# Kernel optimization log

Measured on AMD Instinct MI355X. Metric: run time of the kernel, lower is better.

## Reference

```python
import jax, jax.numpy as jnp
import numpy as np

N_NODES = 50000
N_EDGES = 800000
K_HOPS = 3


def setup_inputs() -> dict:
    key = jax.random.key(0)
    ks = jax.random.split(key, 8)
    x = jax.random.normal(ks[0], (N_NODES, 56), dtype=jnp.float32)
    edge_index = jax.random.randint(ks[1], (2, N_EDGES), 0, N_NODES, dtype=jnp.int64)
    def glorot(k, shape):
        fan_in, fan_out = shape
        s = (6.0 / (fan_in + fan_out)) ** 0.5
        return jax.random.uniform(k, shape, jnp.float32, -s, s)
    return {
        "x": x,
        "edge_index": edge_index,
        "W1": glorot(ks[2], (56, 64)), "b1": jnp.zeros((64,), jnp.float32),
        "W2": glorot(ks[3], (64, 64)), "b2": jnp.zeros((64,), jnp.float32),
        "W3": glorot(ks[4], (64, 64)), "b3": jnp.zeros((64,), jnp.float32),
        "W4": glorot(ks[5], (64, 256)), "b4": jnp.zeros((256,), jnp.float32),
    }


def _gcn_norm(edge_index, num_nodes, dtype):
    # add self loops (PyG SGConv default), then symmetric D^{-1/2}(A+I)D^{-1/2} weights
    loop = jnp.arange(num_nodes, dtype=edge_index.dtype)
    src = jnp.concatenate([edge_index[0], loop])
    dst = jnp.concatenate([edge_index[1], loop])
    deg = jax.ops.segment_sum(jnp.ones_like(src, dtype=dtype), dst, num_segments=num_nodes)
    dinv = jnp.where(deg > 0, jax.lax.rsqrt(deg), 0.0).astype(dtype)
    norm = dinv[src] * dinv[dst]  # [E + N]
    return src, dst, norm


def _propagate_k(h, src, dst, norm, num_nodes, k):
    # k hops of sparse gather-scale-scatter: h <- A_hat @ h
    for _ in range(k):
        h = jax.ops.segment_sum(h[src] * norm[:, None], dst, num_segments=num_nodes)
    return h


def reference(x, edge_index, W1, b1, W2, b2, W3, b3, W4, b4):
    n = x.shape[0]
    src, dst, norm = _gcn_norm(edge_index, n, x.dtype)
    # SGConv layers (dropout is identity in eval mode)
    h = _propagate_k(x, src, dst, norm, n, K_HOPS) @ W1 + b1
    h = _propagate_k(h, src, dst, norm, n, K_HOPS) @ W2 + b2
    h = _propagate_k(h, src, dst, norm, n, K_HOPS) @ W3 + b3
    return h @ W4 + b4  # [N, output]
```

## Files before the change

### kernel.cpp

```cpp
#include <hip/hip_runtime.h>

#define N_NODES 50000
#define N_EDGES 800000
#define F_IN 56
#define F_PAD 64
#define F_OUT 256
#define NB 64
#define ELL_W 64


__global__ void k_fill(const int* __restrict__ ei, int* __restrict__ cnt,
                       int* __restrict__ ell) {
  int e = blockIdx.x * blockDim.x + threadIdx.x;
  if (e >= N_EDGES) return;
  int s = ei[e];
  int d = ei[N_EDGES + e];
  int pos = atomicAdd(&cnt[d], 1);
  ell[(d << 6) + pos] = s;
}


__global__ void k_dinv(const int* __restrict__ cnt, float* __restrict__ dinv,
                       int* __restrict__ deg, int* __restrict__ ell) {
  int i = blockIdx.x * blockDim.x + threadIdx.x;
  if (i >= N_NODES) return;
  int c = cnt[i];
  dinv[i] = rsqrtf((float)(c + 1));
  deg[i] = c + 1;
  ell[(i << 6) + c] = i;
}


__global__ void k_loadx(const float* __restrict__ x, float* __restrict__ h) {
  int i = blockIdx.x * blockDim.x + threadIdx.x;
  int nn = i >> 6, f = i & 63;
  float v = 0.f;
  if (f < F_IN) v = x[nn * F_IN + f];
  else if (f == F_IN) v = 1.f;
  h[i] = v;
}


__global__ __launch_bounds__(256) void k_hop(const float* __restrict__ hin,
                                             float* __restrict__ hout,
                                             const int* __restrict__ deg,
                                             const int* __restrict__ ell,
                                             const float* __restrict__ dinv,
                                             float* __restrict__ vsave) {
  int node = (blockIdx.x * blockDim.x + threadIdx.x) >> 6;
  int lane = threadIdx.x & 63;
  int d = __builtin_amdgcn_readfirstlane(deg[node]);
  int rec = ell[((size_t)node << 6) + lane];
  rec = (lane < d) ? rec : node;
  float dn = __int_as_float(__builtin_amdgcn_readfirstlane(
      __float_as_int(dinv[node])));
  float wl = (lane < d) ? dinv[rec] * dn : 0.f;

  int sub = lane >> 4;
  int fo  = (lane & 15) << 2;
  float4 acc = make_float4(0.f, 0.f, 0.f, 0.f);

  int ngroups = (d + 3) >> 2;
  int g = 0;
  for (; g + 2 <= ngroups; g += 2) {
    int   s0 = __shfl(rec, g * 4 + sub);
    float w0 = __shfl(wl,  g * 4 + sub);
    int   s1 = __shfl(rec, g * 4 + 4 + sub);
    float w1 = __shfl(wl,  g * 4 + 4 + sub);
    float4 a0 = *(const float4*)(hin + (((size_t)s0) << 6) + fo);
    float4 a1 = *(const float4*)(hin + (((size_t)s1) << 6) + fo);
    acc.x = fmaf(w0, a0.x, acc.x);
    acc.y = fmaf(w0, a0.y, acc.y);
    acc.z = fmaf(w0, a0.z, acc.z);
    acc.w = fmaf(w0, a0.w, acc.w);
    acc.x = fmaf(w1, a1.x, acc.x);
    acc.y = fmaf(w1, a1.y, acc.y);
    acc.z = fmaf(w1, a1.z, acc.z);
    acc.w = fmaf(w1, a1.w, acc.w);
  }
  if (g < ngroups) {
    int   s0 = __shfl(rec, g * 4 + sub);
    float w0 = __shfl(wl,  g * 4 + sub);
    float4 a0 = *(const float4*)(hin + (((size_t)s0) << 6) + fo);
    acc.x = fmaf(w0, a0.x, acc.x);
    acc.y = fmaf(w0, a0.y, acc.y);
    acc.z = fmaf(w0, a0.z, acc.z);
    acc.w = fmaf(w0, a0.w, acc.w);
  }
  acc.x += __shfl_xor(acc.x, 16);
  acc.y += __shfl_xor(acc.y, 16);
  acc.z += __shfl_xor(acc.z, 16);
  acc.w += __shfl_xor(acc.w, 16);
  acc.x += __shfl_xor(acc.x, 32);
  acc.y += __shfl_xor(acc.y, 32);
  acc.z += __shfl_xor(acc.z, 32);
  acc.w += __shfl_xor(acc.w, 32);

  if (lane < 16) {
    *(float4*)(hout + ((size_t)node << 6) + fo) = acc;
  }
  if (vsave != nullptr && lane == 14) vsave[node] = acc.x;
}


__global__ void k_weights(const float* __restrict__ W1, const float* __restrict__ b1,
                          const float* __restrict__ W2, const float* __restrict__ b2,
                          const float* __restrict__ W3, const float* __restrict__ b3,
                          const float* __restrict__ W4, const float* __restrict__ b4,
                          float* __restrict__ Mw, float* __restrict__ c1,
                          float* __restrict__ c2, float* __restrict__ c3) {
  __shared__ float t1[64], t2[64], t3[64];
  int m = blockIdx.x, tid = threadIdx.x;
  if (m < F_IN) {
    if (tid < 64) {
      float a = 0.f;
      for (int k = 0; k < 64; ++k) a = fmaf(W1[m * 64 + k], W2[k * 64 + tid], a);
      t1[tid] = a;
    }
    __syncthreads();
    if (tid < 64) {
      float a = 0.f;
      for (int k = 0; k < 64; ++k) a = fmaf(t1[k], W3[k * 64 + tid], a);
      t2[tid] = a;
    }
    __syncthreads();
    {
      float a = 0.f;
      for (int k = 0; k < 64; ++k) a = fmaf(t2[k], W4[k * 256 + tid], a);
      Mw[m * 256 + tid] = a;
    }
  } else {
    if (tid < 64) {
      float a = 0.f;
      for (int k = 0; k < 64; ++k) a = fmaf(b1[k], W2[k * 64 + tid], a);
      t1[tid] = a;
    }
    __syncthreads();
    if (tid < 64) {
      float a = 0.f, b = 0.f;
      for (int k = 0; k < 64; ++k) {
        float w3 = W3[k * 64 + tid];
        a = fmaf(t1[k], w3, a);
        b = fmaf(b2[k], w3, b);
      }
      t2[tid] = a; t3[tid] = b;
    }
    __syncthreads();
    {
      float a = 0.f, b = 0.f, c = 0.f;
      for (int k = 0; k < 64; ++k) {
        float w4 = W4[k * 256 + tid];
        a = fmaf(t2[k], w4, a);
        b = fmaf(t3[k], w4, b);
        c = fmaf(b3[k], w4, c);
      }
      c1[tid] = a; c2[tid] = b; c3[tid] = c + b4[tid];
    }
  }
}


__global__ __launch_bounds__(256) void k_final(const float* __restrict__ y,
                                               const float* __restrict__ v3,
                                               const float* __restrict__ v6,
                                               const float* __restrict__ Mw,
                                               const float* __restrict__ c1,
                                               const float* __restrict__ c2,
                                               const float* __restrict__ c3,
                                               float* __restrict__ out) {
  __shared__ float4 yl[NB][16];
  __shared__ float v3l[NB], v6l[NB];
  int tid = threadIdx.x;
  int j = tid;

  float4 Mreg[14];
#pragma unroll
  for (int k4 = 0; k4 < 14; ++k4) {
    Mreg[k4].x = Mw[(k4 * 4 + 0) * F_OUT + j];
    Mreg[k4].y = Mw[(k4 * 4 + 1) * F_OUT + j];
    Mreg[k4].z = Mw[(k4 * 4 + 2) * F_OUT + j];
    Mreg[k4].w = Mw[(k4 * 4 + 3) * F_OUT + j];
  }
  float C1 = c1[j], C2 = c2[j], C3 = c3[j];

  int n0 = blockIdx.x * NB;
  int lim = min(NB, N_NODES - n0);
  for (int i = tid; i < lim * 16; i += 256) {
    int nn = i >> 4, q = i & 15;
    yl[nn][q] = *(const float4*)(y + ((size_t)(n0 + nn) << 6) + q * 4);
  }
  if (tid < lim) { v3l[tid] = v3[n0 + tid]; v6l[tid] = v6[n0 + tid]; }
  __syncthreads();

  for (int nn = 0; nn < lim; ++nn) {
    float acc = fmaf(v6l[nn], C1, fmaf(v3l[nn], C2, C3));
#pragma unroll
    for (int k4 = 0; k4 < 14; ++k4) {
      float4 yv = yl[nn][k4];
      acc = fmaf(yv.x, Mreg[k4].x, acc);
      acc = fmaf(yv.y, Mreg[k4].y, acc);
      acc = fmaf(yv.z, Mreg[k4].z, acc);
      acc = fmaf(yv.w, Mreg[k4].w, acc);
    }
    out[(size_t)(n0 + nn) * F_OUT + j] = acc;
  }
}


extern "C" void kernel_launch(void* const* d_in, const int* in_sizes, int n_in,
                              void* d_out, int out_size, void* d_ws, size_t ws_size,
                              hipStream_t stream) {
  const float* x  = (const float*)d_in[0];
  const int*   ei = (const int*)d_in[1];
  const float* W1 = (const float*)d_in[2];
  const float* b1 = (const float*)d_in[3];
  const float* W2 = (const float*)d_in[4];
  const float* b2 = (const float*)d_in[5];
  const float* W3 = (const float*)d_in[6];
  const float* b3 = (const float*)d_in[7];
  const float* W4 = (const float*)d_in[8];
  const float* b4 = (const float*)d_in[9];
  float* out = (float*)d_out;

  char* ws = (char*)d_ws;
  size_t off = 0;
  auto take = [&](size_t bytes) -> void* {
    void* p = ws + off;
    off += (bytes + 255) & ~(size_t)255;
    return p;
  };
  int*   cnt   = (int*)take((size_t)N_NODES * 4);
  int*   deg   = (int*)take((size_t)N_NODES * 4);
  float* dinv  = (float*)take((size_t)N_NODES * 4);
  float* v3    = (float*)take((size_t)N_NODES * 4);
  float* v6    = (float*)take((size_t)N_NODES * 4);
  int*   ell   = (int*)take((size_t)N_NODES * ELL_W * 4);
  float* hA    = (float*)take((size_t)N_NODES * F_PAD * 4);
  float* hB    = (float*)take((size_t)N_NODES * F_PAD * 4);
  float* Mw    = (float*)take((size_t)F_IN * F_OUT * 4);
  float* c1    = (float*)take((size_t)F_OUT * 4);
  float* c2    = (float*)take((size_t)F_OUT * 4);
  float* c3    = (float*)take((size_t)F_OUT * 4);

  (void)hipMemsetAsync(cnt, 0, (size_t)N_NODES * 4, stream);
  k_fill<<<(N_EDGES + 255) / 256, 256, 0, stream>>>(ei, cnt, ell);
  k_dinv<<<(N_NODES + 255) / 256, 256, 0, stream>>>(cnt, dinv, deg, ell);
  k_loadx<<<(N_NODES * F_PAD) / 256, 256, 0, stream>>>(x, hA);
  k_weights<<<F_IN + 1, 256, 0, stream>>>(W1, b1, W2, b2, W3, b3, W4, b4, Mw, c1, c2, c3);

  float* src = hA;
  float* dst = hB;
  for (int hop = 1; hop <= 9; ++hop) {
    float* vs = (hop == 3) ? v3 : (hop == 6) ? v6 : nullptr;
    k_hop<<<(N_NODES * F_PAD) / 256, 256, 0, stream>>>(src, dst, deg, ell, dinv, vs);
    float* t = src; src = dst; dst = t;
  }
  k_final<<<(N_NODES + NB - 1) / NB, 256, 0, stream>>>(src, v3, v6, Mw, c1, c2, c3, out);
}
```

Baseline: 386.1 us.

## Partition ELL fill by destination segment, unroll hop gather, dual-row final GEMV

The ELL build now runs as a fixed grid of blocks, each handling only the destination nodes in one of eight segments. This is meant to localise atomics and ELL writes per XCD/cache region, but every block rereads all destination indices. The hop gather loop is unrolled to four neighbour groups so more loads are in flight. The final projection processes two nodes per iteration with split accumulators and halves the block node count to improve ILP and grid size.

```diff
diff --git a/kernel.cpp b/kernel.cpp
--- a/kernel.cpp
+++ b/kernel.cpp
@@ -5,18 +5,26 @@
 #define F_IN 56
 #define F_PAD 64
 #define F_OUT 256
-#define NB 64
+#define NB 32
 #define ELL_W 64
-
-
-__global__ void k_fill(const int* __restrict__ ei, int* __restrict__ cnt,
-                       int* __restrict__ ell) {
-  int e = blockIdx.x * blockDim.x + threadIdx.x;
-  if (e >= N_EDGES) return;
-  int s = ei[e];
-  int d = ei[N_EDGES + e];
-  int pos = atomicAdd(&cnt[d], 1);
-  ell[(d << 6) + pos] = s;
+#define SEG_SZ 6250
+
+
+__global__ __launch_bounds__(256) void k_fill(const int* __restrict__ ei,
+                                              int* __restrict__ cnt,
+                                              int* __restrict__ ell) {
+  int seg = blockIdx.x & 7;
+  int chunk = blockIdx.x >> 3;
+  int nchunks = gridDim.x >> 3;
+  int stride = nchunks * blockDim.x;
+  for (int e = chunk * blockDim.x + threadIdx.x; e < N_EDGES; e += stride) {
+    int d = ei[N_EDGES + e];
+    if (d / SEG_SZ == seg) {
+      int s = ei[e];
+      int pos = atomicAdd(&cnt[d], 1);
+      ell[(d << 6) + pos] = s;
+    }
+  }
 }
 
 
@@ -62,30 +70,34 @@
 
   int ngroups = (d + 3) >> 2;
   int g = 0;
-  for (; g + 2 <= ngroups; g += 2) {
+  for (; g + 4 <= ngroups; g += 4) {
     int   s0 = __shfl(rec, g * 4 + sub);
     float w0 = __shfl(wl,  g * 4 + sub);
     int   s1 = __shfl(rec, g * 4 + 4 + sub);
     float w1 = __shfl(wl,  g * 4 + 4 + sub);
+    int   s2 = __shfl(rec, g * 4 + 8 + sub);
+    float w2 = __shfl(wl,  g * 4 + 8 + sub);
+    int   s3 = __shfl(rec, g * 4 + 12 + sub);
+    float w3 = __shfl(wl,  g * 4 + 12 + sub);
     float4 a0 = *(const float4*)(hin + (((size_t)s0) << 6) + fo);
     float4 a1 = *(const float4*)(hin + (((size_t)s1) << 6) + fo);
-    acc.x = fmaf(w0, a0.x, acc.x);
-    acc.y = fmaf(w0, a0.y, acc.y);
-    acc.z = fmaf(w0, a0.z, acc.z);
-    acc.w = fmaf(w0, a0.w, acc.w);
-    acc.x = fmaf(w1, a1.x, acc.x);
-    acc.y = fmaf(w1, a1.y, acc.y);
-    acc.z = fmaf(w1, a1.z, acc.z);
-    acc.w = fmaf(w1, a1.w, acc.w);
-  }
-  if (g < ngroups) {
+    float4 a2 = *(const float4*)(hin + (((size_t)s2) << 6) + fo);
+    float4 a3 = *(const float4*)(hin + (((size_t)s3) << 6) + fo);
+    acc.x = fmaf(w0, a0.x, acc.x); acc.y = fmaf(w0, a0.y, acc.y);
+    acc.z = fmaf(w0, a0.z, acc.z); acc.w = fmaf(w0, a0.w, acc.w);
+    acc.x = fmaf(w1, a1.x, acc.x); acc.y = fmaf(w1, a1.y, acc.y);
+    acc.z = fmaf(w1, a1.z, acc.z); acc.w = fmaf(w1, a1.w, acc.w);
+    acc.x = fmaf(w2, a2.x, acc.x); acc.y = fmaf(w2, a2.y, acc.y);
+    acc.z = fmaf(w2, a2.z, acc.z); acc.w = fmaf(w2, a2.w, acc.w);
+    acc.x = fmaf(w3, a3.x, acc.x); acc.y = fmaf(w3, a3.y, acc.y);
+    acc.z = fmaf(w3, a3.z, acc.z); acc.w = fmaf(w3, a3.w, acc.w);
+  }
+  for (; g < ngroups; ++g) {
     int   s0 = __shfl(rec, g * 4 + sub);
     float w0 = __shfl(wl,  g * 4 + sub);
     float4 a0 = *(const float4*)(hin + (((size_t)s0) << 6) + fo);
-    acc.x = fmaf(w0, a0.x, acc.x);
-    acc.y = fmaf(w0, a0.y, acc.y);
-    acc.z = fmaf(w0, a0.z, acc.z);
-    acc.w = fmaf(w0, a0.w, acc.w);
+    acc.x = fmaf(w0, a0.x, acc.x); acc.y = fmaf(w0, a0.y, acc.y);
+    acc.z = fmaf(w0, a0.z, acc.z); acc.w = fmaf(w0, a0.w, acc.w);
   }
   acc.x += __shfl_xor(acc.x, 16);
   acc.y += __shfl_xor(acc.y, 16);
@@ -192,17 +204,28 @@
   if (tid < lim) { v3l[tid] = v3[n0 + tid]; v6l[tid] = v6[n0 + tid]; }
   __syncthreads();
 
-  for (int nn = 0; nn < lim; ++nn) {
-    float acc = fmaf(v6l[nn], C1, fmaf(v3l[nn], C2, C3));
+  for (int nn = 0; nn < lim; nn += 2) {
+    bool two = (nn + 1) < lim;
+    float a0 = fmaf(v6l[nn], C1, fmaf(v3l[nn], C2, C3));
+    float a1 = 0.f, a2 = 0.f, a3 = 0.f;
+    int nn2 = two ? nn + 1 : nn;
+    float b0 = fmaf(v6l[nn2], C1, fmaf(v3l[nn2], C2, C3));
+    float b1v = 0.f, b2v = 0.f, b3v = 0.f;
 #pragma unroll
     for (int k4 = 0; k4 < 14; ++k4) {
-      float4 yv = yl[nn][k4];
-      acc = fmaf(yv.x, Mreg[k4].x, acc);
-      acc = fmaf(yv.y, Mreg[k4].y, acc);
-      acc = fmaf(yv.z, Mreg[k4].z, acc);
-      acc = fmaf(yv.w, Mreg[k4].w, acc);
-    }
-    out[(size_t)(n0 + nn) * F_OUT + j] = acc;
+      float4 ya = yl[nn][k4];
+      float4 yb = yl[nn2][k4];
+      a0  = fmaf(ya.x, Mreg[k4].x, a0);
+      a1  = fmaf(ya.y, Mreg[k4].y, a1);
+      a2  = fmaf(ya.z, Mreg[k4].z, a2);
+      a3  = fmaf(ya.w, Mreg[k4].w, a3);
+      b0  = fmaf(yb.x, Mreg[k4].x, b0);
+      b1v = fmaf(yb.y, Mreg[k4].y, b1v);
+      b2v = fmaf(yb.z, Mreg[k4].z, b2v);
+      b3v = fmaf(yb.w, Mreg[k4].w, b3v);
+    }
+    out[(size_t)(n0 + nn) * F_OUT + j] = (a0 + a1) + (a2 + a3);
+    if (two) out[(size_t)(n0 + nn + 1) * F_OUT + j] = (b0 + b1v) + (b2v + b3v);
   }
 }
 
@@ -243,7 +266,7 @@
   float* c3    = (float*)take((size_t)F_OUT * 4);
 
   (void)hipMemsetAsync(cnt, 0, (size_t)N_NODES * 4, stream);
-  k_fill<<<(N_EDGES + 255) / 256, 256, 0, stream>>>(ei, cnt, ell);
+  k_fill<<<1024, 256, 0, stream>>>(ei, cnt, ell);
   k_dinv<<<(N_NODES + 255) / 256, 256, 0, stream>>>(cnt, dinv, deg, ell);
   k_loadx<<<(N_NODES * F_PAD) / 256, 256, 0, stream>>>(x, hA);
   k_weights<<<F_IN + 1, 256, 0, stream>>>(W1, b1, W2, b2, W3, b3, W4, b4, Mw, c1, c2, c3);
```

New measurement: 398.4 us. 3.2% more time.
